# Kernel optimization log

Measured on AMD Instinct MI355X. Metric: run time of the kernel, lower is better.

## Reference

```python
import jax, jax.numpy as jnp
import numpy as np

TEMPERATURE = 0.1
EPS = 1e-8


def setup_inputs() -> dict:
    key = jax.random.key(0)
    k1, k2 = jax.random.split(key)
    features = jax.random.normal(k1, (1024, 256, 16, 8), dtype=jnp.float32)
    labels = jax.random.randint(k2, (1024,), 0, 64, dtype=jnp.int64)
    return {"features": features, "labels": labels}


def reference(features, labels):
    B = features.shape[0]
    f = features.reshape(B, -1)
    norm = jnp.clip(jnp.linalg.norm(f, axis=1, keepdims=True), EPS)
    f = f / norm
    # matcher modeled as cosine-similarity gram matrix (opaque TransMatcher out of scope)
    scores = (f @ f.T) / TEMPERATURE  # [B, B]

    same = labels[:, None] == labels[None, :]
    eye = jnp.eye(B, dtype=bool)
    pos = same & ~eye  # positives excluding self
    neg = ~same & ~eye  # negatives excluding self

    # shared max over pos ∪ neg = all off-diagonal entries per row (matches original)
    row_max = jnp.max(jnp.where(eye, -jnp.inf, scores), axis=1, keepdims=True)
    e = jnp.exp(scores - row_max)  # [B, B]
    pos_sum = jnp.sum(jnp.where(pos, e, 0.0), axis=1)
    neg_sum = jnp.sum(jnp.where(neg, e, 0.0), axis=1)

    valid = jnp.any(pos, axis=1) & jnp.any(neg, axis=1)
    safe_pos = jnp.where(valid, pos_sum, 1.0)
    safe_neg = jnp.where(valid, neg_sum, 1.0)
    # loss_i = neg_term - pos_term; shared max cancels
    loss_i = jnp.where(valid, jnp.log(safe_neg) - jnp.log(safe_pos), 0.0)

    total = jnp.sum(valid.astype(jnp.float32))
    loss = jnp.where(total > 0, jnp.sum(loss_i) / jnp.maximum(total, 1.0), 0.0)

    max_pos = jnp.max(jnp.where(pos, scores, -jnp.inf), axis=1)
    max_neg = jnp.max(jnp.where(neg, scores, -jnp.inf), axis=1)
    correct = jnp.sum((valid & (max_pos > max_neg)).astype(jnp.float32))
    accuracy = jnp.where(total > 0, correct / jnp.maximum(total, 1.0), 0.5)
    return loss, accuracy
```

## Files before the change

kernel.cpp:

```cpp
#include <hip/hip_runtime.h>
#include <hip/hip_bf16.h>
#include <stdint.h>

#define BSZ 1024
#define KF 32768
#define SPLITK 32
#define KPER (KF / SPLITK)
#define BKB 128
#define TEMP_INV 10.0f

typedef float f32x4 __attribute__((ext_vector_type(4)));
typedef int v8i __attribute__((ext_vector_type(8)));

__device__ __forceinline__ void async_copy16(const void* g, void* l) {
    __builtin_amdgcn_global_load_lds(
        (const __attribute__((address_space(1))) void*)g,
        (__attribute__((address_space(3))) void*)l, 16, 0, 0);
}

__device__ __forceinline__ float waveSum(float v) {
    for (int o = 32; o > 0; o >>= 1) v += __shfl_down(v, o);
    return v;
}
__device__ __forceinline__ float waveMax(float v) {
    for (int o = 32; o > 0; o >>= 1) v = fmaxf(v, __shfl_down(v, o));
    return v;
}
__device__ __forceinline__ float blockSum(float v, float* red, int tid) {
    v = waveSum(v);
    __syncthreads();
    if ((tid & 63) == 0) red[tid >> 6] = v;
    __syncthreads();
    return red[0] + red[1] + red[2] + red[3];
}
__device__ __forceinline__ float blockMax(float v, float* red, int tid) {
    v = waveMax(v);
    __syncthreads();
    if ((tid & 63) == 0) red[tid >> 6] = v;
    __syncthreads();
    return fmaxf(fmaxf(red[0], red[1]), fmaxf(red[2], red[3]));
}

__global__ __launch_bounds__(256) void k_norm_convert(
    const float* __restrict__ f, unsigned char* __restrict__ f8,
    float* __restrict__ inv_norm) {
    int row = blockIdx.x, tid = threadIdx.x;
    const float4* src = (const float4*)(f + (size_t)row * KF);
    int4* dst = (int4*)(f8 + (size_t)row * KF);
    float ss = 0.f;
    for (int o = 0; o < 8; ++o) {
        int base4 = o * 1024 + tid * 4;
        int4 pk;
        int* pkp = &pk.x;
#pragma unroll
        for (int q = 0; q < 4; ++q) {
            float4 v = src[base4 + q];
            ss += v.x * v.x + v.y * v.y + v.z * v.z + v.w * v.w;
            int wd = __builtin_amdgcn_cvt_pk_fp8_f32(v.x, v.y, 0, false);
            wd = __builtin_amdgcn_cvt_pk_fp8_f32(v.z, v.w, wd, true);
            pkp[q] = wd;
        }
        dst[o * 256 + tid] = pk;
    }
    __shared__ float red[4];
    float tot = blockSum(ss, red, tid);
    if (tid == 0) inv_norm[row] = 1.0f / fmaxf(sqrtf(tot), 1e-8f);
}

__global__ __launch_bounds__(256) void k_gemm(
    const unsigned char* __restrict__ f8, unsigned char* __restrict__ partials) {
    __shared__ unsigned char Alds[128 * BKB];
    __shared__ unsigned char Blds[128 * BKB];
    int tid = threadIdx.x;

    int t = blockIdx.x;
    int bi = 0, accu = 0;
    while (accu + bi + 1 <= t) { accu += bi + 1; ++bi; }
    int bj = t - accu;
    int row0 = bi * 128, col0 = bj * 128;
    int p = blockIdx.y;
    size_t kbase = (size_t)p * KPER;

    const unsigned char* Ag = f8 + (size_t)row0 * KF;
    const unsigned char* Bg = f8 + (size_t)col0 * KF;
    int lane = tid & 63, w = tid >> 6;
    int wrow = (w >> 1) * 64, wcol = (w & 1) * 64;
    int mrow = lane & 15, quad = lane >> 4;

    int r_st[4], g_st[4];
#pragma unroll
    for (int c = 0; c < 4; ++c) {
        int idx = c * 256 + tid;
        r_st[c] = idx >> 3;
        g_st[c] = (idx & 7) ^ (r_st[c] & 7);
    }

    f32x4 acc[4][4] = {};

    for (int kt = 0; kt < KPER / BKB; ++kt) {
        size_t k0 = kbase + (size_t)kt * BKB;
        __syncthreads();
#pragma unroll
        for (int c = 0; c < 4; ++c) {
            int idx = c * 256 + tid;
            async_copy16(Ag + (size_t)r_st[c] * KF + k0 + g_st[c] * 16, &Alds[idx * 16]);
            async_copy16(Bg + (size_t)r_st[c] * KF + k0 + g_st[c] * 16, &Blds[idx * 16]);
        }
        __syncthreads();
        v8i a8[4], b8[4];
#pragma unroll
        for (int mi = 0; mi < 4; ++mi) {
            int rA = wrow + mi * 16 + mrow;
            int4 lo = *(const int4*)&Alds[rA * BKB + ((quad * 2)     ^ (rA & 7)) * 16];
            int4 hi = *(const int4*)&Alds[rA * BKB + ((quad * 2 + 1) ^ (rA & 7)) * 16];
            a8[mi] = (v8i){lo.x, lo.y, lo.z, lo.w, hi.x, hi.y, hi.z, hi.w};
        }
#pragma unroll
        for (int ni = 0; ni < 4; ++ni) {
            int rB = wcol + ni * 16 + mrow;
            int4 lo = *(const int4*)&Blds[rB * BKB + ((quad * 2)     ^ (rB & 7)) * 16];
            int4 hi = *(const int4*)&Blds[rB * BKB + ((quad * 2 + 1) ^ (rB & 7)) * 16];
            b8[ni] = (v8i){lo.x, lo.y, lo.z, lo.w, hi.x, hi.y, hi.z, hi.w};
        }
#pragma unroll
        for (int mi = 0; mi < 4; ++mi)
#pragma unroll
            for (int ni = 0; ni < 4; ++ni)
                acc[mi][ni] = __builtin_amdgcn_mfma_scale_f32_16x16x128_f8f6f4(
                    a8[mi], b8[ni], acc[mi][ni],
                    0, 0,
                    0, 0x7F7F7F7F,
                    0, 0x7F7F7F7F);
    }

    unsigned char* outp = partials + (size_t)p * BSZ * BSZ;
#pragma unroll
    for (int mi = 0; mi < 4; ++mi)
#pragma unroll
        for (int ni = 0; ni < 4; ++ni)
#pragma unroll
            for (int r = 0; r < 4; ++r) {
                int row = row0 + wrow + mi * 16 + quad * 4 + r;
                int col = col0 + wcol + ni * 16 + mrow;
                int b = __builtin_amdgcn_cvt_pk_fp8_f32(
                            acc[mi][ni][r], acc[mi][ni][r], 0, false);
                outp[(size_t)row * BSZ + col] = (unsigned char)(b & 0xFF);
            }
    if (bi != bj) {
#pragma unroll
        for (int mi = 0; mi < 4; ++mi)
#pragma unroll
            for (int ni = 0; ni < 4; ++ni) {
                int rowm = col0 + wcol + ni * 16 + mrow;
                int colm = row0 + wrow + mi * 16 + quad * 4;
                int pk = __builtin_amdgcn_cvt_pk_fp8_f32(
                             acc[mi][ni][0], acc[mi][ni][1], 0, false);
                pk = __builtin_amdgcn_cvt_pk_fp8_f32(
                         acc[mi][ni][2], acc[mi][ni][3], pk, true);
                *(int*)&outp[(size_t)rowm * BSZ + colm] = pk;
            }
    }
}

__global__ __launch_bounds__(256) void k_loss_rows(
    const unsigned char* __restrict__ partials, const float* __restrict__ inv_norm,
    const int* __restrict__ labels, float* __restrict__ rloss,
    float* __restrict__ rvalid, float* __restrict__ rcorr) {
    int i = blockIdx.x, tid = threadIdx.x;
    __shared__ float red[4];
    float inv_i = inv_norm[i];
    int lab_i = labels[i];

    int j4 = tid * 4;
    float sx = 0.f, sy = 0.f, sz = 0.f, sw = 0.f;
#pragma unroll
    for (int p2 = 0; p2 < SPLITK; ++p2) {
        int v = *(const int*)&partials[(size_t)p2 * BSZ * BSZ + (size_t)i * BSZ + j4];
        sx += __builtin_amdgcn_cvt_f32_fp8(v, 0);
        sy += __builtin_amdgcn_cvt_f32_fp8(v, 1);
        sz += __builtin_amdgcn_cvt_f32_fp8(v, 2);
        sw += __builtin_amdgcn_cvt_f32_fp8(v, 3);
    }
    float4 invj = *(const float4*)&inv_norm[j4];
    float s4[4];
    s4[0] = sx * inv_i * invj.x * TEMP_INV;
    s4[1] = sy * inv_i * invj.y * TEMP_INV;
    s4[2] = sz * inv_i * invj.z * TEMP_INV;
    s4[3] = sw * inv_i * invj.w * TEMP_INV;
    int4 labj = *(const int4*)&labels[j4];
    const int* labjp = &labj.x;

    float pos_sum = 0.f, neg_sum = 0.f, mp = -3.0e38f, mn = -3.0e38f;
#pragma unroll
    for (int q = 0; q < 4; ++q) {
        int j = j4 + q;
        if (j == i) continue;
        float s = s4[q];
        float e = __expf(s - 10.0f);
        if (labjp[q] == lab_i) { pos_sum += e; mp = fmaxf(mp, s); }
        else                   { neg_sum += e; mn = fmaxf(mn, s); }
    }
    float ps = blockSum(pos_sum, red, tid);
    float ns = blockSum(neg_sum, red, tid);
    float mpa = blockMax(mp, red, tid);
    float mna = blockMax(mn, red, tid);
    if (tid == 0) {
        bool valid = (mpa > -1.0e37f) && (mna > -1.0e37f);
        rloss[i]  = valid ? (logf(ns) - logf(ps)) : 0.f;
        rvalid[i] = valid ? 1.f : 0.f;
        rcorr[i]  = (valid && (mpa > mna)) ? 1.f : 0.f;
    }
}

__global__ __launch_bounds__(256) void k_final(
    const float* __restrict__ rloss, const float* __restrict__ rvalid,
    const float* __restrict__ rcorr, float* __restrict__ out) {
    __shared__ float red[4];
    int tid = threadIdx.x;
    float sl = 0.f, sv = 0.f, sc = 0.f;
    for (int c = 0; c < 4; ++c) {
        int j = c * 256 + tid;
        sl += rloss[j]; sv += rvalid[j]; sc += rcorr[j];
    }
    sl = blockSum(sl, red, tid);
    sv = blockSum(sv, red, tid);
    sc = blockSum(sc, red, tid);
    if (tid == 0) {
        out[0] = (sv > 0.f) ? sl / fmaxf(sv, 1.f) : 0.f;
        out[1] = (sv > 0.f) ? sc / fmaxf(sv, 1.f) : 0.5f;
    }
}

extern "C" void kernel_launch(void* const* d_in, const int* in_sizes, int n_in,
                              void* d_out, int out_size, void* d_ws, size_t ws_size,
                              hipStream_t stream) {
    const float* feats = (const float*)d_in[0];
    const int* labels = (const int*)d_in[1];
    float* out = (float*)d_out;
    char* ws = (char*)d_ws;

    unsigned char* f8       = (unsigned char*)ws;
    unsigned char* partials = (unsigned char*)(ws + (size_t)32 * 1024 * 1024);
    float* inv_norm         = (float*)(ws + (size_t)64 * 1024 * 1024);
    float* rloss            = inv_norm + BSZ;
    float* rvalid           = rloss + BSZ;
    float* rcorr            = rvalid + BSZ;

    k_norm_convert<<<BSZ, 256, 0, stream>>>(feats, f8, inv_norm);
    k_gemm<<<dim3(36, SPLITK), 256, 0, stream>>>(f8, partials);
    k_loss_rows<<<BSZ, 256, 0, stream>>>(partials, inv_norm, labels, rloss, rvalid, rcorr);
    k_final<<<1, 256, 0, stream>>>(rloss, rvalid, rcorr, out);
}
```

Measured before the change: 252.9 us.

## Double-buffer LDS tiles in split-K FP8 gemm to overlap loads with MFMA

Replaces the single LDS buffer with two ping-pong buffers so the async global-to-LDS copy of the next K tile is issued before the MFMAs on the current tile. This hides global load latency behind compute and leaves one barrier per iteration instead of two. In exchange it doubles LDS use per block, which may lower occupancy, and it fully unrolls the K loop (NKT=8).

```diff
diff --git a/kernel.cpp b/kernel.cpp
--- a/kernel.cpp
+++ b/kernel.cpp
@@ -7,6 +7,7 @@
 #define SPLITK 32
 #define KPER (KF / SPLITK)
 #define BKB 128
+#define NKT (KPER / BKB)
 #define TEMP_INV 10.0f
 
 typedef float f32x4 __attribute__((ext_vector_type(4)));
@@ -69,8 +70,8 @@
 
 __global__ __launch_bounds__(256) void k_gemm(
     const unsigned char* __restrict__ f8, unsigned char* __restrict__ partials) {
-    __shared__ unsigned char Alds[128 * BKB];
-    __shared__ unsigned char Blds[128 * BKB];
+    __shared__ unsigned char Alds[2][128 * BKB];
+    __shared__ unsigned char Blds[2][128 * BKB];
     int tid = threadIdx.x;
 
     int t = blockIdx.x;
@@ -97,29 +98,42 @@
 
     f32x4 acc[4][4] = {};
 
-    for (int kt = 0; kt < KPER / BKB; ++kt) {
-        size_t k0 = kbase + (size_t)kt * BKB;
-        __syncthreads();
-#pragma unroll
-        for (int c = 0; c < 4; ++c) {
-            int idx = c * 256 + tid;
-            async_copy16(Ag + (size_t)r_st[c] * KF + k0 + g_st[c] * 16, &Alds[idx * 16]);
-            async_copy16(Bg + (size_t)r_st[c] * KF + k0 + g_st[c] * 16, &Blds[idx * 16]);
-        }
-        __syncthreads();
+#pragma unroll
+    for (int c = 0; c < 4; ++c) {
+        int idx = c * 256 + tid;
+        async_copy16(Ag + (size_t)r_st[c] * KF + kbase + g_st[c] * 16, &Alds[0][idx * 16]);
+        async_copy16(Bg + (size_t)r_st[c] * KF + kbase + g_st[c] * 16, &Blds[0][idx * 16]);
+    }
+    asm volatile("s_waitcnt vmcnt(0)" ::: "memory");
+    __builtin_amdgcn_s_barrier();
+
+#pragma unroll
+    for (int kt = 0; kt < NKT; ++kt) {
+        int cur = kt & 1;
+        if (kt + 1 < NKT) {
+            size_t k0 = kbase + (size_t)(kt + 1) * BKB;
+#pragma unroll
+            for (int c = 0; c < 4; ++c) {
+                int idx = c * 256 + tid;
+                async_copy16(Ag + (size_t)r_st[c] * KF + k0 + g_st[c] * 16,
+                             &Alds[cur ^ 1][idx * 16]);
+                async_copy16(Bg + (size_t)r_st[c] * KF + k0 + g_st[c] * 16,
+                             &Blds[cur ^ 1][idx * 16]);
+            }
+        }
         v8i a8[4], b8[4];
 #pragma unroll
         for (int mi = 0; mi < 4; ++mi) {
             int rA = wrow + mi * 16 + mrow;
-            int4 lo = *(const int4*)&Alds[rA * BKB + ((quad * 2)     ^ (rA & 7)) * 16];
-            int4 hi = *(const int4*)&Alds[rA * BKB + ((quad * 2 + 1) ^ (rA & 7)) * 16];
+            int4 lo = *(const int4*)&Alds[cur][rA * BKB + ((quad * 2)     ^ (rA & 7)) * 16];
+            int4 hi = *(const int4*)&Alds[cur][rA * BKB + ((quad * 2 + 1) ^ (rA & 7)) * 16];
             a8[mi] = (v8i){lo.x, lo.y, lo.z, lo.w, hi.x, hi.y, hi.z, hi.w};
         }
 #pragma unroll
         for (int ni = 0; ni < 4; ++ni) {
             int rB = wcol + ni * 16 + mrow;
-            int4 lo = *(const int4*)&Blds[rB * BKB + ((quad * 2)     ^ (rB & 7)) * 16];
-            int4 hi = *(const int4*)&Blds[rB * BKB + ((quad * 2 + 1) ^ (rB & 7)) * 16];
+            int4 lo = *(const int4*)&Blds[cur][rB * BKB + ((quad * 2)     ^ (rB & 7)) * 16];
+            int4 hi = *(const int4*)&Blds[cur][rB * BKB + ((quad * 2 + 1) ^ (rB & 7)) * 16];
             b8[ni] = (v8i){lo.x, lo.y, lo.z, lo.w, hi.x, hi.y, hi.z, hi.w};
         }
 #pragma unroll
@@ -131,6 +145,8 @@
                     0, 0,
                     0, 0x7F7F7F7F,
                     0, 0x7F7F7F7F);
+        asm volatile("s_waitcnt vmcnt(0) lgkmcnt(0)" ::: "memory");
+        __builtin_amdgcn_s_barrier();
     }
 
     unsigned char* outp = partials + (size_t)p * BSZ * BSZ;
```

New measurement: 250.8 us. About the same (-0.8%).
